# Optimization experiments

Measured on AMD Instinct MI355X. Metric: run time of the kernel, lower is better.

## Reference

```python
import jax, jax.numpy as jnp
import numpy as np

EMBED_DIM = 1280
NUM_HEADS = 20
HEAD_DIM = EMBED_DIM // NUM_HEADS
SEQ = 1024
BSZ = 8
ROPE_BASE = 10000.0


def _rope_cos_sin(seq_len, dim, dtype):
    # ESM RotaryEmbedding: inv_freq over even indices, emb = concat(freqs, freqs)
    inv_freq = 1.0 / (ROPE_BASE ** (jnp.arange(0, dim, 2, dtype=jnp.float32) / dim))
    t = jnp.arange(seq_len, dtype=jnp.float32)
    freqs = t[:, None] * inv_freq[None, :]          # [S, D/2]
    emb = jnp.concatenate([freqs, freqs], axis=-1)  # [S, D]
    return jnp.cos(emb).astype(dtype), jnp.sin(emb).astype(dtype)


def _rotate_half(x):
    x1, x2 = jnp.split(x, 2, axis=-1)
    return jnp.concatenate([-x2, x1], axis=-1)


def _apply_rotary(x, cos, sin):
    # x: [B, H, S, D]; cos/sin: [S, D] broadcast over B, H
    return x * cos[None, None, :, :] + _rotate_half(x) * sin[None, None, :, :]


def setup_inputs() -> dict:
    key = jax.random.key(0)
    ks = jax.random.split(key, 9)
    s = 0.02
    return {
        "query": jax.random.normal(ks[0], (SEQ, BSZ, EMBED_DIM), jnp.float32),
        "q_w": jax.random.normal(ks[1], (EMBED_DIM, EMBED_DIM), jnp.float32) * s,
        "q_b": jax.random.normal(ks[2], (EMBED_DIM,), jnp.float32) * s,
        "k_w": jax.random.normal(ks[3], (EMBED_DIM, EMBED_DIM), jnp.float32) * s,
        "k_b": jax.random.normal(ks[4], (EMBED_DIM,), jnp.float32) * s,
        "v_w": jax.random.normal(ks[5], (EMBED_DIM, EMBED_DIM), jnp.float32) * s,
        "v_b": jax.random.normal(ks[6], (EMBED_DIM,), jnp.float32) * s,
        "out_w": jax.random.normal(ks[7], (EMBED_DIM, EMBED_DIM), jnp.float32) * s,
        "out_b": jax.random.normal(ks[8], (EMBED_DIM,), jnp.float32) * s,
    }


def reference(query, q_w, q_b, k_w, k_b, v_w, v_b, out_w, out_b):
    T, B, E = query.shape
    H, D = NUM_HEADS, HEAD_DIM
    scaling = D ** -0.5

    # Separate Q/K/V projections (self-attention: key = value = query)
    q = query @ q_w.T + q_b
    k = query @ k_w.T + k_b
    v = query @ v_w.T + v_b

    # [T, B, E] -> [B, H, T, D]
    def split_heads(x):
        return x.reshape(T, B, H, D).transpose(1, 2, 0, 3)

    q, k, v = split_heads(q), split_heads(k), split_heads(v)

    # Rotary embeddings on q, k
    cos, sin = _rope_cos_sin(T, D, q.dtype)
    q = _apply_rotary(q, cos, sin)
    k = _apply_rotary(k, cos, sin)

    # SDPA with explicit scale = head_dim^-0.5
    scores = jnp.einsum("bhtd,bhsd->bhts", q, k) * scaling
    probs = jax.nn.softmax(scores, axis=-1)
    attn = jnp.einsum("bhts,bhsd->bhtd", probs, v)  # [B, H, T, D]

    # [B, H, T, D] -> [T, B, E]
    attn = attn.transpose(2, 0, 1, 3).reshape(T, B, E)
    return attn @ out_w.T + out_b
```

## Files before the change

kernel.cpp:

```cpp
#include <hip/hip_runtime.h>
#include <math.h>

#define T_SEQ 1024
#define BSZ   8
#define EMB   1280
#define NH    20
#define HD    64
#define MROWS 8192
#define KBYTES (EMB * 2)

typedef __attribute__((ext_vector_type(8))) short bf16x8;
typedef __attribute__((ext_vector_type(4))) float f32x4;

__device__ __forceinline__ short f2bf(float f) {
    unsigned u = __float_as_uint(f);
    u += 0x7fff + ((u >> 16) & 1);
    return (short)(u >> 16);
}
__device__ __forceinline__ float bf2f(short s) {
    return __uint_as_float(((unsigned)(unsigned short)s) << 16);
}

__device__ __forceinline__ void gld16(const void* g, void* l) {
    __builtin_amdgcn_global_load_lds(
        (const __attribute__((address_space(1))) void*)g,
        (__attribute__((address_space(3))) void*)l, 16, 0, 0);
}

__global__ __launch_bounds__(256) void f2bf_kernel(
    const float* __restrict__ in, short* __restrict__ out, int n8)
{
    int i = blockIdx.x * 256 + threadIdx.x;
    if (i >= n8) return;
    const float4* p = (const float4*)in;
    float4 x = p[2 * i], y = p[2 * i + 1];
    bf16x8 o;
    o[0] = f2bf(x.x); o[1] = f2bf(x.y); o[2] = f2bf(x.z); o[3] = f2bf(x.w);
    o[4] = f2bf(y.x); o[5] = f2bf(y.y); o[6] = f2bf(y.z); o[7] = f2bf(y.w);
    ((bf16x8*)out)[i] = o;
}

__global__ void rope_table_kernel(float* __restrict__ cost, float* __restrict__ sint) {
    int idx = blockIdx.x * 256 + threadIdx.x;
    if (idx >= T_SEQ * 32) return;
    int i = idx & 31, t = idx >> 5;
    float inv = powf(10000.0f, -(float)i / 32.0f);
    float f = (float)t * inv;
    cost[idx] = cosf(f);
    sint[idx] = sinf(f);
}

__device__ __forceinline__ void gemm_core(
    const short* __restrict__ A, const short* __restrict__ B,
    char* As, char* Bs, int m0, int n0, int tid, f32x4 (&acc)[4][4])
{
    const int l   = tid & 63;
    const int wid = tid >> 6;
    const int wr  = wid >> 1, wc = wid & 1;

    const int srow = l >> 3;
    const int scol = ((l & 7) ^ srow) << 4;
    const int g16  = (l >> 4) << 4;
    const int swx  = (l & 7) << 4;

    for (int k0 = 0; k0 < EMB; k0 += 64) {
        __syncthreads();
        #pragma unroll
        for (int c = 0; c < 4; ++c) {
            int ch  = wid * 4 + c;
            int row = ch * 8 + srow;
            gld16((const char*)A + (size_t)(m0 + row) * KBYTES + k0 * 2 + scol,
                  As + ch * 1024);
            gld16((const char*)B + (size_t)(n0 + row) * KBYTES + k0 * 2 + scol,
                  Bs + ch * 1024);
        }
        __syncthreads();
        #pragma unroll
        for (int kk = 0; kk < 2; ++kk) {
            const int cb = (kk * 64 + g16) ^ swx;
            bf16x8 af[4], bfr[4];
            #pragma unroll
            for (int m = 0; m < 4; ++m)
                af[m] = *(const bf16x8*)(As + (wr * 64 + m * 16 + (l & 15)) * 128 + cb);
            #pragma unroll
            for (int n = 0; n < 4; ++n)
                bfr[n] = *(const bf16x8*)(Bs + (wc * 64 + n * 16 + (l & 15)) * 128 + cb);
            #pragma unroll
            for (int m = 0; m < 4; ++m)
                #pragma unroll
                for (int n = 0; n < 4; ++n)
                    acc[m][n] = __builtin_amdgcn_mfma_f32_16x16x32_bf16(
                        af[m], bfr[n], acc[m][n], 0, 0, 0);
        }
    }
}

__global__ __launch_bounds__(256) void qkv_gemm_kernel(
    const short* __restrict__ A,
    const short* __restrict__ B0, const short* __restrict__ B1, const short* __restrict__ B2,
    const float* __restrict__ bias0, const float* __restrict__ bias1, const float* __restrict__ bias2,
    short* __restrict__ O0, short* __restrict__ O1, short* __restrict__ O2)
{
    __shared__ short As_s[8192];
    __shared__ short Bs_s[8192];

    const int z = blockIdx.z;
    const short* B = (z == 0) ? B0 : (z == 1) ? B1 : B2;
    const float* bias = (z == 0) ? bias0 : (z == 1) ? bias1 : bias2;
    short* O = (z == 0) ? O0 : (z == 1) ? O1 : O2;
    const float scale = (z == 0) ? 0.125f : 1.0f;

    const int tid = threadIdx.x;
    const int l = tid & 63;
    const int wid = tid >> 6;
    const int wr = wid >> 1, wc = wid & 1;
    const int m0 = blockIdx.x * 128;
    const int n0 = blockIdx.y * 128;

    f32x4 acc[4][4];
    const f32x4 z4 = {0.f, 0.f, 0.f, 0.f};
    #pragma unroll
    for (int m = 0; m < 4; ++m)
        #pragma unroll
        for (int n = 0; n < 4; ++n) acc[m][n] = z4;

    gemm_core(A, B, (char*)As_s, (char*)Bs_s, m0, n0, tid, acc);

    #pragma unroll
    for (int n = 0; n < 4; ++n) {
        int col = n0 + wc * 64 + n * 16 + (l & 15);
        float bv = bias[col];
        int h = col >> 6, d = col & 63;
        #pragma unroll
        for (int m = 0; m < 4; ++m) {
            #pragma unroll
            for (int r = 0; r < 4; ++r) {
                int row = m0 + wr * 64 + m * 16 + (l >> 4) * 4 + r;
                int t = row >> 3, b = row & 7;
                float v = (acc[m][n][r] + bv) * scale;
                O[((size_t)(b * NH + h) * T_SEQ + t) * HD + d] = f2bf(v);
            }
        }
    }
}

__global__ __launch_bounds__(256) void out_gemm_kernel(
    const short* __restrict__ A, const short* __restrict__ B,
    const float* __restrict__ bias, float* __restrict__ O)
{
    __shared__ short As_s[8192];
    __shared__ short Bs_s[8192];

    const int tid = threadIdx.x;
    const int l = tid & 63;
    const int wid = tid >> 6;
    const int wr = wid >> 1, wc = wid & 1;
    const int m0 = blockIdx.x * 128;
    const int n0 = blockIdx.y * 128;

    f32x4 acc[4][4];
    const f32x4 z4 = {0.f, 0.f, 0.f, 0.f};
    #pragma unroll
    for (int m = 0; m < 4; ++m)
        #pragma unroll
        for (int n = 0; n < 4; ++n) acc[m][n] = z4;

    gemm_core(A, B, (char*)As_s, (char*)Bs_s, m0, n0, tid, acc);

    #pragma unroll
    for (int n = 0; n < 4; ++n) {
        int col = n0 + wc * 64 + n * 16 + (l & 15);
        float bv = bias[col];
        #pragma unroll
        for (int m = 0; m < 4; ++m) {
            #pragma unroll
            for (int r = 0; r < 4; ++r) {
                int row = m0 + wr * 64 + m * 16 + (l >> 4) * 4 + r;
                O[(size_t)row * EMB + col] = acc[m][n][r] + bv;
            }
        }
    }
}

__global__ __launch_bounds__(256) void rope_apply_kernel(
    short* __restrict__ q, short* __restrict__ k,
    const float* __restrict__ cost, const float* __restrict__ sint)
{
    int idx = blockIdx.x * 256 + threadIdx.x;
    int i8 = idx & 3;
    int t  = (idx >> 2) & (T_SEQ - 1);
    int bh = idx >> 12;
    size_t base = ((size_t)bh * T_SEQ + t) * HD + i8 * 8;

    float c[8], s[8];
    {
        const float4* cp = (const float4*)(cost + t * 32 + i8 * 8);
        const float4* sp = (const float4*)(sint + t * 32 + i8 * 8);
        float4 c0 = cp[0], c1 = cp[1], s0 = sp[0], s1 = sp[1];
        c[0]=c0.x; c[1]=c0.y; c[2]=c0.z; c[3]=c0.w; c[4]=c1.x; c[5]=c1.y; c[6]=c1.z; c[7]=c1.w;
        s[0]=s0.x; s[1]=s0.y; s[2]=s0.z; s[3]=s0.w; s[4]=s1.x; s[5]=s1.y; s[6]=s1.z; s[7]=s1.w;
    }

    bf16x8 q1 = *(bf16x8*)(q + base), q2 = *(bf16x8*)(q + base + 32);
    bf16x8 k1 = *(bf16x8*)(k + base), k2 = *(bf16x8*)(k + base + 32);
    bf16x8 oq1, oq2, ok1, ok2;
    #pragma unroll
    for (int j = 0; j < 8; ++j) {
        float f1 = bf2f(q1[j]), f2 = bf2f(q2[j]);
        oq1[j] = f2bf(f1 * c[j] - f2 * s[j]);
        oq2[j] = f2bf(f2 * c[j] + f1 * s[j]);
        float g1 = bf2f(k1[j]), g2 = bf2f(k2[j]);
        ok1[j] = f2bf(g1 * c[j] - g2 * s[j]);
        ok2[j] = f2bf(g2 * c[j] + g1 * s[j]);
    }
    *(bf16x8*)(q + base)      = oq1;
    *(bf16x8*)(q + base + 32) = oq2;
    *(bf16x8*)(k + base)      = ok1;
    *(bf16x8*)(k + base + 32) = ok2;
}

__global__ __launch_bounds__(256) void transpose_v_kernel(
    const short* __restrict__ v, short* __restrict__ vt)
{
    __shared__ short tv[64][72];
    const int tid = threadIdx.x;
    const int bh = blockIdx.y, t0 = blockIdx.x * 64;
    const short* src = v + ((size_t)bh * T_SEQ + t0) * HD;
    #pragma unroll
    for (int p = 0; p < 2; ++p) {
        int row = p * 32 + (tid >> 3);
        int c8 = (tid & 7) * 8;
        *(bf16x8*)&tv[row][c8] = *(const bf16x8*)(src + row * HD + c8);
    }
    __syncthreads();
    short* dst = vt + (size_t)bh * (HD * T_SEQ) + t0;
    #pragma unroll
    for (int p = 0; p < 2; ++p) {
        int d = p * 32 + (tid >> 3);
        int t8 = (tid & 7) * 8;
        bf16x8 o;
        #pragma unroll
        for (int j = 0; j < 8; ++j) o[j] = tv[t8 + j][d];
        *(bf16x8*)(dst + (size_t)d * T_SEQ + t8) = o;
    }
}

__global__ __launch_bounds__(256) void attn_kernel(
    const short* __restrict__ Q, const short* __restrict__ K,
    const short* __restrict__ Vt, short* __restrict__ Aout)
{
    __shared__ short Qs_s[4096];
    __shared__ short Ks_s[4096];
    __shared__ short Vs_s[4096];
    __shared__ short Ps_s[4096];
    char* Qs = (char*)Qs_s;
    char* Ks = (char*)Ks_s;
    char* Vs = (char*)Vs_s;
    char* Ps = (char*)Ps_s;

    const int tid = threadIdx.x;
    const int l = tid & 63;
    const int w = tid >> 6;
    const int bh = blockIdx.y;
    const int q0 = blockIdx.x * 64;

    const int srow = l >> 3;
    const int scol = ((l & 7) ^ srow) << 4;
    const int g16  = (l >> 4) << 4;
    const int swx  = (l & 7) << 4;

    const short* Qg = Q + (size_t)bh * (T_SEQ * HD);
    const short* Kg = K + (size_t)bh * (T_SEQ * HD);
    const short* Vg = Vt + (size_t)bh * (HD * T_SEQ);

    #pragma unroll
    for (int c = 0; c < 2; ++c) {
        int ch = w * 2 + c;
        int row = ch * 8 + srow;
        gld16((const char*)Qg + (size_t)(q0 + row) * HD * 2 + scol, Qs + ch * 1024);
    }

    f32x4 oacc[4];
    const f32x4 z4 = {0.f, 0.f, 0.f, 0.f};
    #pragma unroll
    for (int n = 0; n < 4; ++n) oacc[n] = z4;
    float m_i[4], l_i[4];
    #pragma unroll
    for (int r = 0; r < 4; ++r) { m_i[r] = -INFINITY; l_i[r] = 0.f; }

    for (int kt = 0; kt < T_SEQ / 64; ++kt) {
        __syncthreads();
        #pragma unroll
        for (int c = 0; c < 2; ++c) {
            int ch = w * 2 + c;
            int row = ch * 8 + srow;
            gld16((const char*)Kg + (size_t)(kt * 64 + row) * HD * 2 + scol, Ks + ch * 1024);
            gld16((const char*)Vg + ((size_t)row * T_SEQ + kt * 64) * 2 + scol, Vs + ch * 1024);
        }
        __syncthreads();

        f32x4 sacc[4];
        #pragma unroll
        for (int n = 0; n < 4; ++n) sacc[n] = z4;
        #pragma unroll
        for (int kk = 0; kk < 2; ++kk) {
            const int cb = (kk * 64 + g16) ^ swx;
            bf16x8 aq = *(const bf16x8*)(Qs + (w * 16 + (l & 15)) * 128 + cb);
            #pragma unroll
            for (int n = 0; n < 4; ++n) {
                bf16x8 bk = *(const bf16x8*)(Ks + (n * 16 + (l & 15)) * 128 + cb);
                sacc[n] = __builtin_amdgcn_mfma_f32_16x16x32_bf16(aq, bk, sacc[n], 0, 0, 0);
            }
        }

        float corr[4];
        #pragma unroll
        for (int r = 0; r < 4; ++r) {
            float mx = fmaxf(fmaxf(sacc[0][r], sacc[1][r]), fmaxf(sacc[2][r], sacc[3][r]));
            mx = fmaxf(mx, __shfl_xor(mx, 1));
            mx = fmaxf(mx, __shfl_xor(mx, 2));
            mx = fmaxf(mx, __shfl_xor(mx, 4));
            mx = fmaxf(mx, __shfl_xor(mx, 8));
            float mn = fmaxf(m_i[r], mx);
            corr[r] = __expf(m_i[r] - mn);
            m_i[r] = mn;
            int prow = w * 16 + (l >> 4) * 4 + r;
            int pswx = (prow & 7) << 4;
            float rs = 0.f;
            #pragma unroll
            for (int n = 0; n < 4; ++n) {
                float p = __expf(sacc[n][r] - mn);
                rs += p;
                int kv = n * 16 + (l & 15);
                *(short*)(Ps + prow * 128 + ((kv * 2) ^ pswx)) = f2bf(p);
            }
            rs += __shfl_xor(rs, 1);
            rs += __shfl_xor(rs, 2);
            rs += __shfl_xor(rs, 4);
            rs += __shfl_xor(rs, 8);
            l_i[r] = l_i[r] * corr[r] + rs;
        }
        #pragma unroll
        for (int n = 0; n < 4; ++n) {
            f32x4 o = oacc[n];
            o[0] *= corr[0]; o[1] *= corr[1]; o[2] *= corr[2]; o[3] *= corr[3];
            oacc[n] = o;
        }

        #pragma unroll
        for (int kk = 0; kk < 2; ++kk) {
            const int cb = (kk * 64 + g16) ^ swx;
            bf16x8 ap = *(const bf16x8*)(Ps + (w * 16 + (l & 15)) * 128 + cb);
            #pragma unroll
            for (int n = 0; n < 4; ++n) {
                bf16x8 bv = *(const bf16x8*)(Vs + (n * 16 + (l & 15)) * 128 + cb);
                oacc[n] = __builtin_amdgcn_mfma_f32_16x16x32_bf16(ap, bv, oacc[n], 0, 0, 0);
            }
        }
    }

    const int b_ = bh / NH, h = bh % NH;
    #pragma unroll
    for (int n = 0; n < 4; ++n) {
        int d = h * HD + n * 16 + (l & 15);
        #pragma unroll
        for (int r = 0; r < 4; ++r) {
            int t = q0 + w * 16 + (l >> 4) * 4 + r;
            float v = oacc[n][r] / l_i[r];
            Aout[((size_t)t * BSZ + b_) * EMB + d] = f2bf(v);
        }
    }
}

extern "C" void kernel_launch(void* const* d_in, const int* in_sizes, int n_in,
                              void* d_out, int out_size, void* d_ws, size_t ws_size,
                              hipStream_t stream) {
    const float* X     = (const float*)d_in[0];
    const float* q_w   = (const float*)d_in[1];
    const float* q_b   = (const float*)d_in[2];
    const float* k_w   = (const float*)d_in[3];
    const float* k_b   = (const float*)d_in[4];
    const float* v_w   = (const float*)d_in[5];
    const float* v_b   = (const float*)d_in[6];
    const float* out_w = (const float*)d_in[7];
    const float* out_b = (const float*)d_in[8];
    float* out = (float*)d_out;

    short* ws = (short*)d_ws;
    const size_t NACT = (size_t)MROWS * EMB;
    const size_t NW   = (size_t)EMB * EMB;
    short* xb  = ws;
    short* wqb = xb + NACT;
    short* wkb = wqb + NW;
    short* wvb = wkb + NW;
    short* wob = wvb + NW;
    short* qb  = wob + NW;
    short* kb  = qb + NACT;
    short* vb  = kb + NACT;
    short* vtb = vb + NACT;
    short* ab  = vtb + NACT;
    float* cost = (float*)(ab + NACT);
    float* sint = cost + T_SEQ * 32;

    rope_table_kernel<<<dim3(128), 256, 0, stream>>>(cost, sint);
    f2bf_kernel<<<dim3(5120), 256, 0, stream>>>(X, xb, (int)(NACT / 8));
    f2bf_kernel<<<dim3(800), 256, 0, stream>>>(q_w, wqb, (int)(NW / 8));
    f2bf_kernel<<<dim3(800), 256, 0, stream>>>(k_w, wkb, (int)(NW / 8));
    f2bf_kernel<<<dim3(800), 256, 0, stream>>>(v_w, wvb, (int)(NW / 8));
    f2bf_kernel<<<dim3(800), 256, 0, stream>>>(out_w, wob, (int)(NW / 8));

    qkv_gemm_kernel<<<dim3(MROWS / 128, EMB / 128, 3), 256, 0, stream>>>(
        xb, wqb, wkb, wvb, q_b, k_b, v_b, qb, kb, vb);

    rope_apply_kernel<<<dim3(2560), 256, 0, stream>>>(qb, kb, cost, sint);

    transpose_v_kernel<<<dim3(T_SEQ / 64, BSZ * NH), 256, 0, stream>>>(vb, vtb);

    attn_kernel<<<dim3(T_SEQ / 64, BSZ * NH), 256, 0, stream>>>(qb, kb, vtb, ab);

    out_gemm_kernel<<<dim3(MROWS / 128, EMB / 128), 256, 0, stream>>>(
        ab, wob, out_b, out);
}
```

Before: 445.3 us.

## Fuse RoPE into QKV GEMM epilogue, double-buffer attention K/V, batch weight casts

Applies rotary embedding to Q and K inside the QKV GEMM epilogue while the values are still fp32 in registers. This removes the separate rope_apply pass, which read and wrote Q and K again. The attention kernel now double-buffers K/V tiles in LDS so the next tile loads during compute, raises wave priority around the MFMA blocks, and swizzles the block-to-(q,bh) mapping. The four weight-cast launches are merged into one, at the cost of doubled LDS in attention, which may lower occupancy.

```diff
diff --git a/kernel.cpp b/kernel.cpp
--- a/kernel.cpp
+++ b/kernel.cpp
@@ -40,6 +40,25 @@
     ((bf16x8*)out)[i] = o;
 }
 
+__global__ __launch_bounds__(256) void wcast_kernel(
+    const float* __restrict__ w0, const float* __restrict__ w1,
+    const float* __restrict__ w2, const float* __restrict__ w3,
+    short* __restrict__ o0, short* __restrict__ o1,
+    short* __restrict__ o2, short* __restrict__ o3, int n8)
+{
+    int which = blockIdx.y;
+    const float* in = (which == 0) ? w0 : (which == 1) ? w1 : (which == 2) ? w2 : w3;
+    short* out      = (which == 0) ? o0 : (which == 1) ? o1 : (which == 2) ? o2 : o3;
+    int i = blockIdx.x * 256 + threadIdx.x;
+    if (i >= n8) return;
+    const float4* p = (const float4*)in;
+    float4 x = p[2 * i], y = p[2 * i + 1];
+    bf16x8 o;
+    o[0] = f2bf(x.x); o[1] = f2bf(x.y); o[2] = f2bf(x.z); o[3] = f2bf(x.w);
+    o[4] = f2bf(y.x); o[5] = f2bf(y.y); o[6] = f2bf(y.z); o[7] = f2bf(y.w);
+    ((bf16x8*)out)[i] = o;
+}
+
 __global__ void rope_table_kernel(float* __restrict__ cost, float* __restrict__ sint) {
     int idx = blockIdx.x * 256 + threadIdx.x;
     if (idx >= T_SEQ * 32) return;
@@ -99,6 +118,7 @@
     const short* __restrict__ A,
     const short* __restrict__ B0, const short* __restrict__ B1, const short* __restrict__ B2,
     const float* __restrict__ bias0, const float* __restrict__ bias1, const float* __restrict__ bias2,
+    const float* __restrict__ cost, const float* __restrict__ sint,
     short* __restrict__ O0, short* __restrict__ O1, short* __restrict__ O2)
 {
     __shared__ short As_s[8192];
@@ -130,6 +150,35 @@
     for (int n = 0; n < 4; ++n) {
         int col = n0 + wc * 64 + n * 16 + (l & 15);
         float bv = bias[col];
+        #pragma unroll
+        for (int m = 0; m < 4; ++m)
+            #pragma unroll
+            for (int r = 0; r < 4; ++r) acc[m][n][r] += bv;
+    }
+
+    if (z < 2) {
+        #pragma unroll
+        for (int m = 0; m < 4; ++m) {
+            #pragma unroll
+            for (int r = 0; r < 4; ++r) {
+                int row = m0 + wr * 64 + m * 16 + (l >> 4) * 4 + r;
+                int t = row >> 3;
+                #pragma unroll
+                for (int n = 0; n < 2; ++n) {
+                    int i = n * 16 + (l & 15);
+                    float c = cost[t * 32 + i];
+                    float s = sint[t * 32 + i];
+                    float x1 = acc[m][n][r], x2 = acc[m][n + 2][r];
+                    acc[m][n][r]     = x1 * c - x2 * s;
+                    acc[m][n + 2][r] = x2 * c + x1 * s;
+                }
+            }
+        }
+    }
+
+    #pragma unroll
+    for (int n = 0; n < 4; ++n) {
+        int col = n0 + wc * 64 + n * 16 + (l & 15);
         int h = col >> 6, d = col & 63;
         #pragma unroll
         for (int m = 0; m < 4; ++m) {
@@ -137,8 +186,7 @@
             for (int r = 0; r < 4; ++r) {
                 int row = m0 + wr * 64 + m * 16 + (l >> 4) * 4 + r;
                 int t = row >> 3, b = row & 7;
-                float v = (acc[m][n][r] + bv) * scale;
-                O[((size_t)(b * NH + h) * T_SEQ + t) * HD + d] = f2bf(v);
+                O[((size_t)(b * NH + h) * T_SEQ + t) * HD + d] = f2bf(acc[m][n][r] * scale);
             }
         }
     }
@@ -182,43 +230,6 @@
     }
 }
 
-__global__ __launch_bounds__(256) void rope_apply_kernel(
-    short* __restrict__ q, short* __restrict__ k,
-    const float* __restrict__ cost, const float* __restrict__ sint)
-{
-    int idx = blockIdx.x * 256 + threadIdx.x;
-    int i8 = idx & 3;
-    int t  = (idx >> 2) & (T_SEQ - 1);
-    int bh = idx >> 12;
-    size_t base = ((size_t)bh * T_SEQ + t) * HD + i8 * 8;
-
-    float c[8], s[8];
-    {
-        const float4* cp = (const float4*)(cost + t * 32 + i8 * 8);
-        const float4* sp = (const float4*)(sint + t * 32 + i8 * 8);
-        float4 c0 = cp[0], c1 = cp[1], s0 = sp[0], s1 = sp[1];
-        c[0]=c0.x; c[1]=c0.y; c[2]=c0.z; c[3]=c0.w; c[4]=c1.x; c[5]=c1.y; c[6]=c1.z; c[7]=c1.w;
-        s[0]=s0.x; s[1]=s0.y; s[2]=s0.z; s[3]=s0.w; s[4]=s1.x; s[5]=s1.y; s[6]=s1.z; s[7]=s1.w;
-    }
-
-    bf16x8 q1 = *(bf16x8*)(q + base), q2 = *(bf16x8*)(q + base + 32);
-    bf16x8 k1 = *(bf16x8*)(k + base), k2 = *(bf16x8*)(k + base + 32);
-    bf16x8 oq1, oq2, ok1, ok2;
-    #pragma unroll
-    for (int j = 0; j < 8; ++j) {
-        float f1 = bf2f(q1[j]), f2 = bf2f(q2[j]);
-        oq1[j] = f2bf(f1 * c[j] - f2 * s[j]);
-        oq2[j] = f2bf(f2 * c[j] + f1 * s[j]);
-        float g1 = bf2f(k1[j]), g2 = bf2f(k2[j]);
-        ok1[j] = f2bf(g1 * c[j] - g2 * s[j]);
-        ok2[j] = f2bf(g2 * c[j] + g1 * s[j]);
-    }
-    *(bf16x8*)(q + base)      = oq1;
-    *(bf16x8*)(q + base + 32) = oq2;
-    *(bf16x8*)(k + base)      = ok1;
-    *(bf16x8*)(k + base + 32) = ok2;
-}
-
 __global__ __launch_bounds__(256) void transpose_v_kernel(
     const short* __restrict__ v, short* __restrict__ vt)
 {
@@ -250,8 +261,8 @@
     const short* __restrict__ Vt, short* __restrict__ Aout)
 {
     __shared__ short Qs_s[4096];
-    __shared__ short Ks_s[4096];
-    __shared__ short Vs_s[4096];
+    __shared__ short Ks_s[8192];
+    __shared__ short Vs_s[8192];
     __shared__ short Ps_s[4096];
     char* Qs = (char*)Qs_s;
     char* Ks = (char*)Ks_s;
@@ -261,8 +272,11 @@
     const int tid = threadIdx.x;
     const int l = tid & 63;
     const int w = tid >> 6;
-    const int bh = blockIdx.y;
-    const int q0 = blockIdx.x * 64;
+
+    const int bid = blockIdx.y * 16 + blockIdx.x;
+    const int swz = (bid & 7) * 320 + (bid >> 3);
+    const int q0 = (swz & 15) * 64;
+    const int bh = swz >> 4;
 
     const int srow = l >> 3;
     const int scol = ((l & 7) ^ srow) << 4;
@@ -278,7 +292,10 @@
         int ch = w * 2 + c;
         int row = ch * 8 + srow;
         gld16((const char*)Qg + (size_t)(q0 + row) * HD * 2 + scol, Qs + ch * 1024);
-    }
+        gld16((const char*)Kg + (size_t)(row) * HD * 2 + scol, Ks + ch * 1024);
+        gld16((const char*)Vg + ((size_t)row * T_SEQ) * 2 + scol, Vs + ch * 1024);
+    }
+    __syncthreads();
 
     f32x4 oacc[4];
     const f32x4 z4 = {0.f, 0.f, 0.f, 0.f};
@@ -288,30 +305,37 @@
     #pragma unroll
     for (int r = 0; r < 4; ++r) { m_i[r] = -INFINITY; l_i[r] = 0.f; }
 
+    int buf = 0;
     for (int kt = 0; kt < T_SEQ / 64; ++kt) {
-        __syncthreads();
-        #pragma unroll
-        for (int c = 0; c < 2; ++c) {
-            int ch = w * 2 + c;
-            int row = ch * 8 + srow;
-            gld16((const char*)Kg + (size_t)(kt * 64 + row) * HD * 2 + scol, Ks + ch * 1024);
-            gld16((const char*)Vg + ((size_t)row * T_SEQ + kt * 64) * 2 + scol, Vs + ch * 1024);
-        }
-        __syncthreads();
+        if (kt + 1 < T_SEQ / 64) {
+            const int ob = (buf ^ 1) * 8192;
+            #pragma unroll
+            for (int c = 0; c < 2; ++c) {
+                int ch = w * 2 + c;
+                int row = ch * 8 + srow;
+                gld16((const char*)Kg + (size_t)((kt + 1) * 64 + row) * HD * 2 + scol,
+                      Ks + ob + ch * 1024);
+                gld16((const char*)Vg + ((size_t)row * T_SEQ + (kt + 1) * 64) * 2 + scol,
+                      Vs + ob + ch * 1024);
+            }
+        }
+        const int cbuf = buf * 8192;
 
         f32x4 sacc[4];
         #pragma unroll
         for (int n = 0; n < 4; ++n) sacc[n] = z4;
+        __builtin_amdgcn_s_setprio(1);
         #pragma unroll
         for (int kk = 0; kk < 2; ++kk) {
             const int cb = (kk * 64 + g16) ^ swx;
             bf16x8 aq = *(const bf16x8*)(Qs + (w * 16 + (l & 15)) * 128 + cb);
             #pragma unroll
             for (int n = 0; n < 4; ++n) {
-                bf16x8 bk = *(const bf16x8*)(Ks + (n * 16 + (l & 15)) * 128 + cb);
+                bf16x8 bk = *(const bf16x8*)(Ks + cbuf + (n * 16 + (l & 15)) * 128 + cb);
                 sacc[n] = __builtin_amdgcn_mfma_f32_16x16x32_bf16(aq, bk, sacc[n], 0, 0, 0);
             }
         }
+        __builtin_amdgcn_s_setprio(0);
 
         float corr[4];
         #pragma unroll
@@ -347,16 +371,21 @@
             oacc[n] = o;
         }
 
+        __builtin_amdgcn_s_setprio(1);
         #pragma unroll
         for (int kk = 0; kk < 2; ++kk) {
             const int cb = (kk * 64 + g16) ^ swx;
             bf16x8 ap = *(const bf16x8*)(Ps + (w * 16 + (l & 15)) * 128 + cb);
             #pragma unroll
             for (int n = 0; n < 4; ++n) {
-                bf16x8 bv = *(const bf16x8*)(Vs + (n * 16 + (l & 15)) * 128 + cb);
+                bf16x8 bv = *(const bf16x8*)(Vs + cbuf + (n * 16 + (l & 15)) * 128 + cb);
                 oacc[n] = __builtin_amdgcn_mfma_f32_16x16x32_bf16(ap, bv, oacc[n], 0, 0, 0);
             }
         }
+        __builtin_amdgcn_s_setprio(0);
+
+        __syncthreads();
+        buf ^= 1;
     }
 
     const int b_ = bh / NH, h = bh % NH;
@@ -404,15 +433,11 @@
 
     rope_table_kernel<<<dim3(128), 256, 0, stream>>>(cost, sint);
     f2bf_kernel<<<dim3(5120), 256, 0, stream>>>(X, xb, (int)(NACT / 8));
-    f2bf_kernel<<<dim3(800), 256, 0, stream>>>(q_w, wqb, (int)(NW / 8));
-    f2bf_kernel<<<dim3(800), 256, 0, stream>>>(k_w, wkb, (int)(NW / 8));
-    f2bf_kernel<<<dim3(800), 256, 0, stream>>>(v_w, wvb, (int)(NW / 8));
-    f2bf_kernel<<<dim3(800), 256, 0, stream>>>(out_w, wob, (int)(NW / 8));
+    wcast_kernel<<<dim3(800, 4), 256, 0, stream>>>(
+        q_w, k_w, v_w, out_w, wqb, wkb, wvb, wob, (int)(NW / 8));
 
     qkv_gemm_kernel<<<dim3(MROWS / 128, EMB / 128, 3), 256, 0, stream>>>(
-        xb, wqb, wkb, wvb, q_b, k_b, v_b, qb, kb, vb);
-
-    rope_apply_kernel<<<dim3(2560), 256, 0, stream>>>(qb, kb, cost, sint);
+        xb, wqb, wkb, wvb, q_b, k_b, v_b, cost, sint, qb, kb, vb);
 
     transpose_v_kernel<<<dim3(T_SEQ / 64, BSZ * NH), 256, 0, stream>>>(vb, vtb);
 
```

After: 427.8 us. 1.04x faster.
